# Kernel tuning notes

Hardware: AMD Instinct MI355X
Metric: run time of the kernel (lower is better)

The kernel has to match this reference:

```python
import jax, jax.numpy as jnp
import numpy as np

DIM = 256
WINDOW = 8
NUM_HEADS = 8
N = WINDOW * WINDOW  # tokens per window
HEAD_DIM = DIM // NUM_HEADS
SCALE = HEAD_DIM ** -0.5
B_ = 2048


def _relative_position_index(w):
    coords = np.stack(np.meshgrid(np.arange(w), np.arange(w), indexing='ij'))  # 2,w,w
    cf = coords.reshape(2, -1)  # 2,N
    rel = cf[:, :, None] - cf[:, None, :]  # 2,N,N
    rel = rel.transpose(1, 2, 0) + (w - 1)  # N,N,2 in [0, 2w-2]
    return rel[..., 0] * (2 * w - 1) + rel[..., 1]  # N,N

REL_INDEX = jnp.asarray(_relative_position_index(WINDOW))  # (N,N) int


def setup_inputs() -> dict:
    key = jax.random.key(0)
    ks = jax.random.split(key, 8)
    x = jax.random.normal(ks[0], (B_, N, DIM), dtype=jnp.float32)
    mask = jax.random.normal(ks[1], (B_, 1, N, N), dtype=jnp.float32)
    w_qkv = jax.random.normal(ks[2], (3 * DIM, DIM), dtype=jnp.float32) * (DIM ** -0.5)
    b_qkv = jnp.zeros((3 * DIM,), dtype=jnp.float32)
    w_proj = jax.random.normal(ks[3], (DIM, DIM), dtype=jnp.float32) * (DIM ** -0.5)
    b_proj = jnp.zeros((DIM,), dtype=jnp.float32)
    bias_table = jax.random.normal(ks[4], ((2 * WINDOW - 1) ** 2, NUM_HEADS), dtype=jnp.float32) * 0.02
    return {"x": x, "mask": mask, "w_qkv": w_qkv, "b_qkv": b_qkv,
            "w_proj": w_proj, "b_proj": b_proj, "bias_table": bias_table}


def reference(x, mask, w_qkv, b_qkv, w_proj, b_proj, bias_table):
    Bw, n, c = x.shape
    qkv = x @ w_qkv.T + b_qkv  # (B_, N, 3*C)
    qkv = qkv.reshape(Bw, n, 3, NUM_HEADS, HEAD_DIM)
    q = qkv[:, :, 0].transpose(0, 2, 1, 3) * SCALE  # (B_, H, N, hd)
    k = qkv[:, :, 1].transpose(0, 2, 1, 3)
    v = qkv[:, :, 2].transpose(0, 2, 1, 3)
    attn = jnp.einsum('bhnd,bhmd->bhnm', q, k)  # (B_, H, N, N)
    rel_bias = bias_table[REL_INDEX]  # (N, N, H)
    attn = attn + rel_bias.transpose(2, 0, 1)[None]  # broadcast (1,H,N,N)
    attn = attn + mask  # (B_,1,N,N) broadcasts over heads
    attn = jax.nn.softmax(attn, axis=-1)
    out = jnp.einsum('bhnm,bhmd->bhnd', attn, v)  # (B_, H, N, hd)
    out = out.transpose(0, 2, 1, 3).reshape(Bw, n, c)
    return out @ w_proj.T + b_proj
```

## Files before the change

kernel.cpp:

```cpp
#include <hip/hip_runtime.h>

#define NWIN 2048
#define NTOK 64
#define CDIM 256
#define NH 8
#define HD 32
#define QSCALE 0.17677669529663689f

#define LDA 264
#define LDQ 36
#define LDV 72
#define LDP 68

typedef __bf16 bf16x4 __attribute__((ext_vector_type(4)));
typedef __bf16 bf16x8 __attribute__((ext_vector_type(8)));
typedef float  f32x4  __attribute__((ext_vector_type(4)));

__device__ __forceinline__ unsigned short f2bf(float f) {
    union { float f; unsigned u; } v; v.f = f;
    unsigned r = v.u + 0x7FFFu + ((v.u >> 16) & 1u);
    return (unsigned short)(r >> 16);
}

__device__ __forceinline__ bf16x8 ld16(const unsigned short* p) {
    return *(const bf16x8*)p;
}
__device__ __forceinline__ bf16x8 ld8u(const unsigned short* p) {
    bf16x4 lo = *(const bf16x4*)p;
    bf16x4 hi = *(const bf16x4*)(p + 4);
    return __builtin_shufflevector(lo, hi, 0, 1, 2, 3, 4, 5, 6, 7);
}

__global__ void precast_kernel(const float* __restrict__ wq, const float* __restrict__ wp,
                               const float* __restrict__ bt,
                               unsigned short* __restrict__ wqb, unsigned short* __restrict__ wpb,
                               float* __restrict__ relbT) {
    int i = blockIdx.x * 256 + threadIdx.x;
    if (i < 196608) {
        wqb[i] = f2bf(wq[i]);
    } else if (i < 262144) {
        wpb[i - 196608] = f2bf(wp[i - 196608]);
    } else if (i < 294912) {
        int j = i - 262144;
        int h = j >> 12;
        int c = (j >> 6) & 63;
        int r = j & 63;
        int yi = r >> 3, xi = r & 7, yj = c >> 3, xj = c & 7;
        int idx = (yi - yj + 7) * 15 + (xi - xj + 7);
        relbT[j] = bt[idx * NH + h];
    }
}

__global__ __launch_bounds__(512, 2)
void win_attn_kernel(const float* __restrict__ x, const float* __restrict__ mask,
                     const float* __restrict__ bq, const float* __restrict__ bp,
                     const unsigned short* __restrict__ wq, const unsigned short* __restrict__ wp,
                     const float* __restrict__ relbT, float* __restrict__ out) {
    __shared__ __align__(16) unsigned short sm[80896];
    unsigned short* sA = sm;
    unsigned short* sQ = sm + 16896;
    unsigned short* sK = sm + 35328;
    unsigned short* sV = sm + 53760;
    unsigned short* sP = sm + 72192;

    const int b    = blockIdx.x;
    const int tid  = threadIdx.x;
    const int wv   = tid >> 6;
    const int lane = tid & 63;
    const int lm   = lane & 15;
    const int quad = lane >> 4;
    const f32x4 fzero = {0.f, 0.f, 0.f, 0.f};

    {
        const int row = tid >> 3;
        const int c0  = (tid & 7) * 32;
        const float4* gx = (const float4*)(x + ((size_t)b * NTOK + row) * CDIM + c0);
        unsigned short* dst = sA + row * LDA + c0;
        #pragma unroll
        for (int i = 0; i < 8; ++i) {
            float4 v = gx[i];
            ushort4 u;
            u.x = f2bf(v.x); u.y = f2bf(v.y); u.z = f2bf(v.z); u.w = f2bf(v.w);
            *(ushort4*)(dst + i * 4) = u;
        }
    }
    __syncthreads();

    {
        const int h = wv;
        const int nbase[6] = { h*HD, h*HD + 16,
                               CDIM + h*HD, CDIM + h*HD + 16,
                               2*CDIM + h*HD, 2*CDIM + h*HD + 16 };
        f32x4 acc[4][6];
        #pragma unroll
        for (int mt = 0; mt < 4; ++mt)
            #pragma unroll
            for (int t = 0; t < 6; ++t) acc[mt][t] = fzero;

        #pragma unroll
        for (int ks = 0; ks < 8; ++ks) {
            bf16x8 bfr[6];
            #pragma unroll
            for (int t = 0; t < 6; ++t)
                bfr[t] = ld16(wq + (nbase[t] + lm) * CDIM + ks * 32 + quad * 8);
            bf16x8 afr[4];
            #pragma unroll
            for (int mt = 0; mt < 4; ++mt)
                afr[mt] = ld16(sA + (mt * 16 + lm) * LDA + ks * 32 + quad * 8);
            #pragma unroll
            for (int mt = 0; mt < 4; ++mt)
                #pragma unroll
                for (int t = 0; t < 6; ++t)
                    acc[mt][t] = __builtin_amdgcn_mfma_f32_16x16x32_bf16(afr[mt], bfr[t], acc[mt][t], 0, 0, 0);
        }

        float bqv[6];
        #pragma unroll
        for (int t = 0; t < 6; ++t) bqv[t] = bq[nbase[t] + lm];

        unsigned short* sQh = sQ + h * (NTOK * LDQ);
        unsigned short* sKh = sK + h * (NTOK * LDQ);
        unsigned short* sVh = sV + h * (HD * LDV);
        #pragma unroll
        for (int mt = 0; mt < 4; ++mt) {
            #pragma unroll
            for (int t = 0; t < 6; ++t) {
                #pragma unroll
                for (int reg = 0; reg < 4; ++reg) {
                    float val = acc[mt][t][reg] + bqv[t];
                    int tok = mt * 16 + quad * 4 + reg;
                    if (t < 2)      sQh[tok * LDQ + t * 16 + lm]          = f2bf(val * QSCALE);
                    else if (t < 4) sKh[tok * LDQ + (t - 2) * 16 + lm]    = f2bf(val);
                    else            sVh[((t - 4) * 16 + lm) * LDV + tok]  = f2bf(val);
                }
            }
        }
    }
    __syncthreads();

    {
        const int h = wv;
        const unsigned short* sQh = sQ + h * (NTOK * LDQ);
        const unsigned short* sKh = sK + h * (NTOK * LDQ);
        const unsigned short* sVh = sV + h * (HD * LDV);
        unsigned short* sPh = sP + wv * (16 * LDP);

        bf16x8 kf[4];
        #pragma unroll
        for (int jt = 0; jt < 4; ++jt)
            kf[jt] = ld8u(sKh + (jt * 16 + lm) * LDQ + quad * 8);
        bf16x8 vf[2][2];
        #pragma unroll
        for (int nt = 0; nt < 2; ++nt)
            #pragma unroll
            for (int kk = 0; kk < 2; ++kk)
                vf[nt][kk] = ld16(sVh + (nt * 16 + lm) * LDV + kk * 32 + quad * 8);

        const float* maskb = mask + (size_t)b * (NTOK * NTOK);
        const float* relh  = relbT + h * (NTOK * NTOK);

        for (int rc = 0; rc < 4; ++rc) {
            const int m0 = rc * 16;
            bf16x8 qa = ld8u(sQh + (m0 + lm) * LDQ + quad * 8);
            f32x4 s[4];
            #pragma unroll
            for (int jt = 0; jt < 4; ++jt)
                s[jt] = __builtin_amdgcn_mfma_f32_16x16x32_bf16(qa, kf[jt], fzero, 0, 0, 0);

            #pragma unroll
            for (int jt = 0; jt < 4; ++jt) {
                float4 rb4 = *(const float4*)(relh + (jt * 16 + lm) * 64 + m0 + quad * 4);
                float rbv[4] = { rb4.x, rb4.y, rb4.z, rb4.w };
                #pragma unroll
                for (int reg = 0; reg < 4; ++reg) {
                    int r = m0 + quad * 4 + reg;
                    s[jt][reg] += rbv[reg] + maskb[r * 64 + jt * 16 + lm];
                }
            }

            float mx[4], inv[4];
            #pragma unroll
            for (int reg = 0; reg < 4; ++reg) {
                float m_ = fmaxf(fmaxf(s[0][reg], s[1][reg]), fmaxf(s[2][reg], s[3][reg]));
                #pragma unroll
                for (int off = 1; off < 16; off <<= 1)
                    m_ = fmaxf(m_, __shfl_xor(m_, off, 64));
                mx[reg] = m_;
            }
            float p[4][4];
            #pragma unroll
            for (int jt = 0; jt < 4; ++jt)
                #pragma unroll
                for (int reg = 0; reg < 4; ++reg)
                    p[jt][reg] = __expf(s[jt][reg] - mx[reg]);
            #pragma unroll
            for (int reg = 0; reg < 4; ++reg) {
                float s_ = (p[0][reg] + p[1][reg]) + (p[2][reg] + p[3][reg]);
                #pragma unroll
                for (int off = 1; off < 16; off <<= 1)
                    s_ += __shfl_xor(s_, off, 64);
                inv[reg] = 1.0f / s_;
            }

            #pragma unroll
            for (int jt = 0; jt < 4; ++jt)
                #pragma unroll
                for (int reg = 0; reg < 4; ++reg)
                    sPh[(quad * 4 + reg) * LDP + jt * 16 + lm] = f2bf(p[jt][reg]);

            bf16x8 pa0 = ld8u(sPh + lm * LDP + quad * 8);
            bf16x8 pa1 = ld8u(sPh + lm * LDP + 32 + quad * 8);
            #pragma unroll
            for (int nt = 0; nt < 2; ++nt) {
                f32x4 o = __builtin_amdgcn_mfma_f32_16x16x32_bf16(pa0, vf[nt][0], fzero, 0, 0, 0);
                o = __builtin_amdgcn_mfma_f32_16x16x32_bf16(pa1, vf[nt][1], o, 0, 0, 0);
                #pragma unroll
                for (int reg = 0; reg < 4; ++reg) {
                    int r = m0 + quad * 4 + reg;
                    sA[r * LDA + h * HD + nt * 16 + lm] = f2bf(o[reg] * inv[reg]);
                }
            }
        }
    }
    __syncthreads();

    {
        const int n0 = wv * HD;
        f32x4 acc[4][2];
        #pragma unroll
        for (int mt = 0; mt < 4; ++mt) { acc[mt][0] = fzero; acc[mt][1] = fzero; }

        #pragma unroll
        for (int ks = 0; ks < 8; ++ks) {
            bf16x8 bfr[2];
            #pragma unroll
            for (int nt = 0; nt < 2; ++nt)
                bfr[nt] = ld16(wp + (n0 + nt * 16 + lm) * CDIM + ks * 32 + quad * 8);
            bf16x8 afr[4];
            #pragma unroll
            for (int mt = 0; mt < 4; ++mt)
                afr[mt] = ld16(sA + (mt * 16 + lm) * LDA + ks * 32 + quad * 8);
            #pragma unroll
            for (int mt = 0; mt < 4; ++mt)
                #pragma unroll
                for (int nt = 0; nt < 2; ++nt)
                    acc[mt][nt] = __builtin_amdgcn_mfma_f32_16x16x32_bf16(afr[mt], bfr[nt], acc[mt][nt], 0, 0, 0);
        }

        float bpv[2] = { bp[n0 + lm], bp[n0 + 16 + lm] };
        #pragma unroll
        for (int mt = 0; mt < 4; ++mt)
            #pragma unroll
            for (int nt = 0; nt < 2; ++nt)
                #pragma unroll
                for (int reg = 0; reg < 4; ++reg) {
                    int r = mt * 16 + quad * 4 + reg;
                    out[((size_t)b * NTOK + r) * CDIM + n0 + nt * 16 + lm] = acc[mt][nt][reg] + bpv[nt];
                }
    }
}

extern "C" void kernel_launch(void* const* d_in, const int* in_sizes, int n_in,
                              void* d_out, int out_size, void* d_ws, size_t ws_size,
                              hipStream_t stream) {
    const float* x    = (const float*)d_in[0];
    const float* mask = (const float*)d_in[1];
    const float* wq   = (const float*)d_in[2];
    const float* bq   = (const float*)d_in[3];
    const float* wp   = (const float*)d_in[4];
    const float* bp   = (const float*)d_in[5];
    const float* bt   = (const float*)d_in[6];

    unsigned short* wqb   = (unsigned short*)d_ws;
    unsigned short* wpb   = wqb + 196608;
    float*          relbT = (float*)((char*)d_ws + 524288);
    float*          out   = (float*)d_out;

    precast_kernel<<<1152, 256, 0, stream>>>(wq, wp, bt, wqb, wpb, relbT);
    win_attn_kernel<<<NWIN, 512, 0, stream>>>(x, mask, bq, bp, wqb, wpb, relbT, out);
}
```

Measured before the change: 435.2 us.

## Keep Q/K/V and probabilities in registers via permlane swaps, shrink LDS

Computes Q and K transposed (weights as A operand) and V normally, then uses v_cvt_pk_bf16_f32 with permlane32/16 swaps to reshape MFMA accumulators directly into operand fragments. Q, K, V and P no longer round-trip through LDS, the intermediate barrier is removed, and S is computed transposed so the softmax row reduction needs only two cross-lane shuffles and the mask/bias loads become float4. LDS drops to two 64x264 bf16 buffers and launch bounds go to 4 blocks per CU to raise occupancy. The risk is register pressure under the tighter bound, and correctness depends on the permlane lane mapping.

```diff
diff --git a/kernel.cpp b/kernel.cpp
--- a/kernel.cpp
+++ b/kernel.cpp
@@ -8,13 +8,10 @@
 #define QSCALE 0.17677669529663689f
 
 #define LDA 264
-#define LDQ 36
-#define LDV 72
-#define LDP 68
-
-typedef __bf16 bf16x4 __attribute__((ext_vector_type(4)));
+
 typedef __bf16 bf16x8 __attribute__((ext_vector_type(8)));
 typedef float  f32x4  __attribute__((ext_vector_type(4)));
+typedef unsigned int u32x4 __attribute__((ext_vector_type(4)));
 
 __device__ __forceinline__ unsigned short f2bf(float f) {
     union { float f; unsigned u; } v; v.f = f;
@@ -25,16 +22,37 @@
 __device__ __forceinline__ bf16x8 ld16(const unsigned short* p) {
     return *(const bf16x8*)p;
 }
-__device__ __forceinline__ bf16x8 ld8u(const unsigned short* p) {
-    bf16x4 lo = *(const bf16x4*)p;
-    bf16x4 hi = *(const bf16x4*)(p + 4);
-    return __builtin_shufflevector(lo, hi, 0, 1, 2, 3, 4, 5, 6, 7);
+
+__device__ __forceinline__ unsigned cvtpk(float lo, float hi) {
+    unsigned r;
+    asm("v_cvt_pk_bf16_f32 %0, %1, %2" : "=v"(r) : "v"(lo), "v"(hi));
+    return r;
+}
+__device__ __forceinline__ void pl32(unsigned &a, unsigned &b) {
+    asm("v_permlane32_swap_b32 %0, %1" : "+v"(a), "+v"(b));
+}
+__device__ __forceinline__ void pl16(unsigned &a, unsigned &b) {
+    asm("v_permlane16_swap_b32 %0, %1" : "+v"(a), "+v"(b));
+}
+
+__device__ __forceinline__ bf16x8 xchg32(f32x4 t0, f32x4 t1) {
+    unsigned u00 = cvtpk(t0[0], t0[1]);
+    unsigned u01 = cvtpk(t0[2], t0[3]);
+    unsigned u10 = cvtpk(t1[0], t1[1]);
+    unsigned u11 = cvtpk(t1[2], t1[3]);
+    pl32(u00, u10);
+    pl32(u01, u11);
+    pl16(u00, u10);
+    pl16(u01, u11);
+    union { u32x4 u; bf16x8 v; } r;
+    r.u = (u32x4){u00, u01, u10, u11};
+    return r.v;
 }
 
 __global__ void precast_kernel(const float* __restrict__ wq, const float* __restrict__ wp,
                                const float* __restrict__ bt,
                                unsigned short* __restrict__ wqb, unsigned short* __restrict__ wpb,
-                               float* __restrict__ relbT) {
+                               float* __restrict__ relbQ) {
     int i = blockIdx.x * 256 + threadIdx.x;
     if (i < 196608) {
         wqb[i] = f2bf(wq[i]);
@@ -43,25 +61,22 @@
     } else if (i < 294912) {
         int j = i - 262144;
         int h = j >> 12;
-        int c = (j >> 6) & 63;
-        int r = j & 63;
-        int yi = r >> 3, xi = r & 7, yj = c >> 3, xj = c & 7;
-        int idx = (yi - yj + 7) * 15 + (xi - xj + 7);
-        relbT[j] = bt[idx * NH + h];
-    }
-}
-
-__global__ __launch_bounds__(512, 2)
+        int q = (j >> 6) & 63;
+        int k = j & 63;
+        int yq = q >> 3, xq = q & 7, yk = k >> 3, xk = k & 7;
+        int idx = (yq - yk + 7) * 15 + (xq - xk + 7);
+        relbQ[j] = bt[idx * NH + h];
+    }
+}
+
+__global__ __launch_bounds__(512, 4)
 void win_attn_kernel(const float* __restrict__ x, const float* __restrict__ mask,
                      const float* __restrict__ bq, const float* __restrict__ bp,
                      const unsigned short* __restrict__ wq, const unsigned short* __restrict__ wp,
-                     const float* __restrict__ relbT, float* __restrict__ out) {
-    __shared__ __align__(16) unsigned short sm[80896];
+                     const float* __restrict__ relbQ, float* __restrict__ out) {
+    __shared__ __align__(16) unsigned short sm[2 * NTOK * LDA];
     unsigned short* sA = sm;
-    unsigned short* sQ = sm + 16896;
-    unsigned short* sK = sm + 35328;
-    unsigned short* sV = sm + 53760;
-    unsigned short* sP = sm + 72192;
+    unsigned short* sO = sm + NTOK * LDA;
 
     const int b    = blockIdx.x;
     const int tid  = threadIdx.x;
@@ -77,149 +92,158 @@
         const float4* gx = (const float4*)(x + ((size_t)b * NTOK + row) * CDIM + c0);
         unsigned short* dst = sA + row * LDA + c0;
         #pragma unroll
-        for (int i = 0; i < 8; ++i) {
-            float4 v = gx[i];
-            ushort4 u;
-            u.x = f2bf(v.x); u.y = f2bf(v.y); u.z = f2bf(v.z); u.w = f2bf(v.w);
-            *(ushort4*)(dst + i * 4) = u;
+        for (int i = 0; i < 4; ++i) {
+            float4 a = gx[2 * i];
+            float4 c = gx[2 * i + 1];
+            u32x4 w = { cvtpk(a.x, a.y), cvtpk(a.z, a.w), cvtpk(c.x, c.y), cvtpk(c.z, c.w) };
+            *(u32x4*)(dst + i * 8) = w;
         }
     }
     __syncthreads();
 
-    {
-        const int h = wv;
-        const int nbase[6] = { h*HD, h*HD + 16,
-                               CDIM + h*HD, CDIM + h*HD + 16,
-                               2*CDIM + h*HD, 2*CDIM + h*HD + 16 };
-        f32x4 acc[4][6];
+    const int h = wv;
+
+    bf16x8 qf[4];
+    bf16x8 kf[4];
+    {
+        f32x4 qk[4][4];
+        #pragma unroll
+        for (int ft = 0; ft < 4; ++ft)
+            #pragma unroll
+            for (int nt = 0; nt < 4; ++nt) qk[ft][nt] = fzero;
+
+        const int fb[4] = { h*HD, h*HD + 16, CDIM + h*HD, CDIM + h*HD + 16 };
+        #pragma unroll
+        for (int ks = 0; ks < 8; ++ks) {
+            bf16x8 xa[4], wf[4];
+            #pragma unroll
+            for (int nt = 0; nt < 4; ++nt)
+                xa[nt] = ld16(sA + (nt * 16 + lm) * LDA + ks * 32 + quad * 8);
+            #pragma unroll
+            for (int ft = 0; ft < 4; ++ft)
+                wf[ft] = ld16(wq + (fb[ft] + lm) * CDIM + ks * 32 + quad * 8);
+            #pragma unroll
+            for (int ft = 0; ft < 4; ++ft)
+                #pragma unroll
+                for (int nt = 0; nt < 4; ++nt)
+                    qk[ft][nt] = __builtin_amdgcn_mfma_f32_16x16x32_bf16(wf[ft], xa[nt], qk[ft][nt], 0, 0, 0);
+        }
+
+        const float4 bQ0 = *(const float4*)(bq + h*HD + quad*4);
+        const float4 bQ1 = *(const float4*)(bq + h*HD + 16 + quad*4);
+        const float4 bK0 = *(const float4*)(bq + CDIM + h*HD + quad*4);
+        const float4 bK1 = *(const float4*)(bq + CDIM + h*HD + 16 + quad*4);
+        const float q0v[4] = {bQ0.x, bQ0.y, bQ0.z, bQ0.w};
+        const float q1v[4] = {bQ1.x, bQ1.y, bQ1.z, bQ1.w};
+        const float k0v[4] = {bK0.x, bK0.y, bK0.z, bK0.w};
+        const float k1v[4] = {bK1.x, bK1.y, bK1.z, bK1.w};
+
+        #pragma unroll
+        for (int nt = 0; nt < 4; ++nt) {
+            #pragma unroll
+            for (int r = 0; r < 4; ++r) {
+                qk[0][nt][r] = (qk[0][nt][r] + q0v[r]) * QSCALE;
+                qk[1][nt][r] = (qk[1][nt][r] + q1v[r]) * QSCALE;
+                qk[2][nt][r] += k0v[r];
+                qk[3][nt][r] += k1v[r];
+            }
+            qf[nt] = xchg32(qk[0][nt], qk[1][nt]);
+            kf[nt] = xchg32(qk[2][nt], qk[3][nt]);
+        }
+    }
+
+    bf16x8 vf[2][2];
+    {
+        f32x4 va[4][2];
+        #pragma unroll
+        for (int mt = 0; mt < 4; ++mt) { va[mt][0] = fzero; va[mt][1] = fzero; }
+
+        #pragma unroll
+        for (int ks = 0; ks < 8; ++ks) {
+            bf16x8 xa[4], wfv[2];
+            #pragma unroll
+            for (int mt = 0; mt < 4; ++mt)
+                xa[mt] = ld16(sA + (mt * 16 + lm) * LDA + ks * 32 + quad * 8);
+            #pragma unroll
+            for (int t = 0; t < 2; ++t)
+                wfv[t] = ld16(wq + (2*CDIM + h*HD + t*16 + lm) * CDIM + ks * 32 + quad * 8);
+            #pragma unroll
+            for (int mt = 0; mt < 4; ++mt)
+                #pragma unroll
+                for (int t = 0; t < 2; ++t)
+                    va[mt][t] = __builtin_amdgcn_mfma_f32_16x16x32_bf16(xa[mt], wfv[t], va[mt][t], 0, 0, 0);
+        }
+
+        const float bV0 = bq[2*CDIM + h*HD + lm];
+        const float bV1 = bq[2*CDIM + h*HD + 16 + lm];
         #pragma unroll
         for (int mt = 0; mt < 4; ++mt)
             #pragma unroll
-            for (int t = 0; t < 6; ++t) acc[mt][t] = fzero;
-
-        #pragma unroll
-        for (int ks = 0; ks < 8; ++ks) {
-            bf16x8 bfr[6];
-            #pragma unroll
-            for (int t = 0; t < 6; ++t)
-                bfr[t] = ld16(wq + (nbase[t] + lm) * CDIM + ks * 32 + quad * 8);
-            bf16x8 afr[4];
-            #pragma unroll
-            for (int mt = 0; mt < 4; ++mt)
-                afr[mt] = ld16(sA + (mt * 16 + lm) * LDA + ks * 32 + quad * 8);
-            #pragma unroll
-            for (int mt = 0; mt < 4; ++mt)
-                #pragma unroll
-                for (int t = 0; t < 6; ++t)
-                    acc[mt][t] = __builtin_amdgcn_mfma_f32_16x16x32_bf16(afr[mt], bfr[t], acc[mt][t], 0, 0, 0);
-        }
-
-        float bqv[6];
-        #pragma unroll
-        for (int t = 0; t < 6; ++t) bqv[t] = bq[nbase[t] + lm];
-
-        unsigned short* sQh = sQ + h * (NTOK * LDQ);
-        unsigned short* sKh = sK + h * (NTOK * LDQ);
-        unsigned short* sVh = sV + h * (HD * LDV);
-        #pragma unroll
-        for (int mt = 0; mt < 4; ++mt) {
-            #pragma unroll
-            for (int t = 0; t < 6; ++t) {
-                #pragma unroll
-                for (int reg = 0; reg < 4; ++reg) {
-                    float val = acc[mt][t][reg] + bqv[t];
-                    int tok = mt * 16 + quad * 4 + reg;
-                    if (t < 2)      sQh[tok * LDQ + t * 16 + lm]          = f2bf(val * QSCALE);
-                    else if (t < 4) sKh[tok * LDQ + (t - 2) * 16 + lm]    = f2bf(val);
-                    else            sVh[((t - 4) * 16 + lm) * LDV + tok]  = f2bf(val);
+            for (int r = 0; r < 4; ++r) { va[mt][0][r] += bV0; va[mt][1][r] += bV1; }
+
+        #pragma unroll
+        for (int t = 0; t < 2; ++t)
+            #pragma unroll
+            for (int kk = 0; kk < 2; ++kk)
+                vf[t][kk] = xchg32(va[2*kk][t], va[2*kk + 1][t]);
+    }
+
+    {
+        const float* maskb = mask + (size_t)b * (NTOK * NTOK);
+        const float* relh  = relbQ + h * (NTOK * NTOK);
+
+        #pragma unroll
+        for (int rc = 0; rc < 4; ++rc) {
+            f32x4 s[4];
+            #pragma unroll
+            for (int jt = 0; jt < 4; ++jt)
+                s[jt] = __builtin_amdgcn_mfma_f32_16x16x32_bf16(kf[jt], qf[rc], fzero, 0, 0, 0);
+
+            const float* mrow = maskb + (rc * 16 + lm) * 64;
+            const float* rrow = relh  + (rc * 16 + lm) * 64;
+            #pragma unroll
+            for (int jt = 0; jt < 4; ++jt) {
+                float4 rb = *(const float4*)(rrow + jt * 16 + quad * 4);
+                float4 mk = *(const float4*)(mrow + jt * 16 + quad * 4);
+                const float rbv[4] = {rb.x, rb.y, rb.z, rb.w};
+                const float mkv[4] = {mk.x, mk.y, mk.z, mk.w};
+                #pragma unroll
+                for (int r = 0; r < 4; ++r) s[jt][r] += rbv[r] + mkv[r];
+            }
+
+            float mx = s[0][0];
+            #pragma unroll
+            for (int jt = 0; jt < 4; ++jt)
+                #pragma unroll
+                for (int r = 0; r < 4; ++r) mx = fmaxf(mx, s[jt][r]);
+            mx = fmaxf(mx, __shfl_xor(mx, 16, 64));
+            mx = fmaxf(mx, __shfl_xor(mx, 32, 64));
+
+            float sum = 0.f;
+            #pragma unroll
+            for (int jt = 0; jt < 4; ++jt)
+                #pragma unroll
+                for (int r = 0; r < 4; ++r) {
+                    float e = __expf(s[jt][r] - mx);
+                    s[jt][r] = e;
+                    sum += e;
                 }
-            }
-        }
-    }
-    __syncthreads();
-
-    {
-        const int h = wv;
-        const unsigned short* sQh = sQ + h * (NTOK * LDQ);
-        const unsigned short* sKh = sK + h * (NTOK * LDQ);
-        const unsigned short* sVh = sV + h * (HD * LDV);
-        unsigned short* sPh = sP + wv * (16 * LDP);
-
-        bf16x8 kf[4];
-        #pragma unroll
-        for (int jt = 0; jt < 4; ++jt)
-            kf[jt] = ld8u(sKh + (jt * 16 + lm) * LDQ + quad * 8);
-        bf16x8 vf[2][2];
-        #pragma unroll
-        for (int nt = 0; nt < 2; ++nt)
-            #pragma unroll
-            for (int kk = 0; kk < 2; ++kk)
-                vf[nt][kk] = ld16(sVh + (nt * 16 + lm) * LDV + kk * 32 + quad * 8);
-
-        const float* maskb = mask + (size_t)b * (NTOK * NTOK);
-        const float* relh  = relbT + h * (NTOK * NTOK);
-
-        for (int rc = 0; rc < 4; ++rc) {
-            const int m0 = rc * 16;
-            bf16x8 qa = ld8u(sQh + (m0 + lm) * LDQ + quad * 8);
-            f32x4 s[4];
-            #pragma unroll
-            for (int jt = 0; jt < 4; ++jt)
-                s[jt] = __builtin_amdgcn_mfma_f32_16x16x32_bf16(qa, kf[jt], fzero, 0, 0, 0);
-
-            #pragma unroll
-            for (int jt = 0; jt < 4; ++jt) {
-                float4 rb4 = *(const float4*)(relh + (jt * 16 + lm) * 64 + m0 + quad * 4);
-                float rbv[4] = { rb4.x, rb4.y, rb4.z, rb4.w };
-                #pragma unroll
-                for (int reg = 0; reg < 4; ++reg) {
-                    int r = m0 + quad * 4 + reg;
-                    s[jt][reg] += rbv[reg] + maskb[r * 64 + jt * 16 + lm];
-                }
-            }
-
-            float mx[4], inv[4];
-            #pragma unroll
-            for (int reg = 0; reg < 4; ++reg) {
-                float m_ = fmaxf(fmaxf(s[0][reg], s[1][reg]), fmaxf(s[2][reg], s[3][reg]));
-                #pragma unroll
-                for (int off = 1; off < 16; off <<= 1)
-                    m_ = fmaxf(m_, __shfl_xor(m_, off, 64));
-                mx[reg] = m_;
-            }
-            float p[4][4];
-            #pragma unroll
-            for (int jt = 0; jt < 4; ++jt)
-                #pragma unroll
-                for (int reg = 0; reg < 4; ++reg)
-                    p[jt][reg] = __expf(s[jt][reg] - mx[reg]);
-            #pragma unroll
-            for (int reg = 0; reg < 4; ++reg) {
-                float s_ = (p[0][reg] + p[1][reg]) + (p[2][reg] + p[3][reg]);
-                #pragma unroll
-                for (int off = 1; off < 16; off <<= 1)
-                    s_ += __shfl_xor(s_, off, 64);
-                inv[reg] = 1.0f / s_;
-            }
-
-            #pragma unroll
-            for (int jt = 0; jt < 4; ++jt)
-                #pragma unroll
-                for (int reg = 0; reg < 4; ++reg)
-                    sPh[(quad * 4 + reg) * LDP + jt * 16 + lm] = f2bf(p[jt][reg]);
-
-            bf16x8 pa0 = ld8u(sPh + lm * LDP + quad * 8);
-            bf16x8 pa1 = ld8u(sPh + lm * LDP + 32 + quad * 8);
-            #pragma unroll
-            for (int nt = 0; nt < 2; ++nt) {
-                f32x4 o = __builtin_amdgcn_mfma_f32_16x16x32_bf16(pa0, vf[nt][0], fzero, 0, 0, 0);
-                o = __builtin_amdgcn_mfma_f32_16x16x32_bf16(pa1, vf[nt][1], o, 0, 0, 0);
-                #pragma unroll
-                for (int reg = 0; reg < 4; ++reg) {
-                    int r = m0 + quad * 4 + reg;
-                    sA[r * LDA + h * HD + nt * 16 + lm] = f2bf(o[reg] * inv[reg]);
-                }
-            }
+            sum += __shfl_xor(sum, 16, 64);
+            sum += __shfl_xor(sum, 32, 64);
+            const float inv = 1.0f / sum;
+
+            bf16x8 pb0 = xchg32(s[0], s[1]);
+            bf16x8 pb1 = xchg32(s[2], s[3]);
+
+            f32x4 o0 = __builtin_amdgcn_mfma_f32_16x16x32_bf16(vf[0][0], pb0, fzero, 0, 0, 0);
+            o0 = __builtin_amdgcn_mfma_f32_16x16x32_bf16(vf[0][1], pb1, o0, 0, 0, 0);
+            f32x4 o1 = __builtin_amdgcn_mfma_f32_16x16x32_bf16(vf[1][0], pb0, fzero, 0, 0, 0);
+            o1 = __builtin_amdgcn_mfma_f32_16x16x32_bf16(vf[1][1], pb1, o1, 0, 0, 0);
+            #pragma unroll
+            for (int r = 0; r < 4; ++r) { o0[r] *= inv; o1[r] *= inv; }
+
+            bf16x8 ob = xchg32(o0, o1);
+            *(bf16x8*)(sO + (rc * 16 + lm) * LDA + h * HD + quad * 8) = ob;
         }
     }
     __syncthreads();
@@ -239,7 +263,7 @@
             bf16x8 afr[4];
             #pragma unroll
             for (int mt = 0; mt < 4; ++mt)
-                afr[mt] = ld16(sA + (mt * 16 + lm) * LDA + ks * 32 + quad * 8);
+                afr[mt] = ld16(sO + (mt * 16 + lm) * LDA + ks * 32 + quad * 8);
             #pragma unroll
             for (int mt = 0; mt < 4; ++mt)
                 #pragma unroll
@@ -273,9 +297,9 @@
 
     unsigned short* wqb   = (unsigned short*)d_ws;
     unsigned short* wpb   = wqb + 196608;
-    float*          relbT = (float*)((char*)d_ws + 524288);
+    float*          relbQ = (float*)((char*)d_ws + 524288);
     float*          out   = (float*)d_out;
 
-    precast_kernel<<<1152, 256, 0, stream>>>(wq, wp, bt, wqb, wpb, relbT);
-    win_attn_kernel<<<NWIN, 512, 0, stream>>>(x, mask, bq, bp, wqb, wpb, relbT, out);
-}
+    precast_kernel<<<1152, 256, 0, stream>>>(wq, wp, bt, wqb, wpb, relbQ);
+    win_attn_kernel<<<NWIN, 512, 0, stream>>>(x, mask, bq, bp, wqb, wpb, relbQ, out);
+}
```

After: 599.4 us. +37.7%, slower.
